# Optimization experiments

Hardware: AMD Instinct MI355X
Metric: run time of the kernel (lower is better)

The kernel has to match this reference:

```python
import jax, jax.numpy as jnp
import numpy as np


def setup_inputs() -> dict:
    key = jax.random.key(0)
    k1, k2 = jax.random.split(key)
    # output packs [mean; diagonal_covariance] along dim 0 (torch.chunk(output, 2))
    output = jax.random.uniform(k1, (8192, 2048), dtype=jnp.float32, minval=0.05, maxval=1.0)
    target = jax.random.uniform(k2, (4096, 2048), dtype=jnp.float32)
    return {"output": output, "target": target}


def reference(output, target):
    mean, diag_cov = jnp.split(output, 2, axis=0)          # each [B, D]
    mean_err = mean - target
    # logdet(diagflat(cov)) == sum(log(cov)) over ALL entries (diagflat flattens) -> scalar
    logdet = jnp.sum(jnp.log(diag_cov))
    loss = mean_err * mean_err / diag_cov + logdet          # scalar broadcasts
    return -loss
```

## Files before the change

### kernel.cpp

```cpp
#include <hip/hip_runtime.h>


#define N_ELEMS (4096 * 2048)
#define N_VEC4  (N_ELEMS / 4)
#define NBLK    2048
#define NTHR    256
#define ITERS   (N_VEC4 / (NBLK * NTHR))

__global__ __launch_bounds__(256) void logdet_partial_kernel(
    const float* __restrict__ cov, float* __restrict__ partials) {
    const float4* __restrict__ c4 = reinterpret_cast<const float4*>(cov);
    int idx = blockIdx.x * blockDim.x + threadIdx.x;
    const int stride = NBLK * NTHR;

    float s = 0.0f;
    #pragma unroll
    for (int it = 0; it < ITERS; ++it) {
        float4 v = c4[idx + it * stride];
        s += __logf(v.x) + __logf(v.y) + __logf(v.z) + __logf(v.w);
    }

    #pragma unroll
    for (int off = 32; off > 0; off >>= 1)
        s += __shfl_down(s, off, 64);

    __shared__ float wsum[4];
    if ((threadIdx.x & 63) == 0) wsum[threadIdx.x >> 6] = s;
    __syncthreads();
    if (threadIdx.x == 0)
        partials[blockIdx.x] = wsum[0] + wsum[1] + wsum[2] + wsum[3];
}

__global__ __launch_bounds__(256) void nll_elem_kernel(
    const float* __restrict__ mean, const float* __restrict__ cov,
    const float* __restrict__ target, const float* __restrict__ partials,
    float* __restrict__ out) {
    const float4* __restrict__ p4 = reinterpret_cast<const float4*>(partials);
    float4 pa = p4[threadIdx.x];
    float4 pb = p4[threadIdx.x + 256];
    float s = (pa.x + pa.y) + (pa.z + pa.w) + (pb.x + pb.y) + (pb.z + pb.w);
    #pragma unroll
    for (int off = 32; off > 0; off >>= 1)
        s += __shfl_down(s, off, 64);
    __shared__ float wsum[4];
    if ((threadIdx.x & 63) == 0) wsum[threadIdx.x >> 6] = s;
    __syncthreads();
    const float logdet = (wsum[0] + wsum[1]) + (wsum[2] + wsum[3]);

    const float4* __restrict__ m4 = reinterpret_cast<const float4*>(mean);
    const float4* __restrict__ c4 = reinterpret_cast<const float4*>(cov);
    const float4* __restrict__ t4 = reinterpret_cast<const float4*>(target);
    float4* __restrict__ o4 = reinterpret_cast<float4*>(out);

    int idx = blockIdx.x * blockDim.x + threadIdx.x;
    const int stride = NBLK * NTHR;

    #pragma unroll
    for (int it = 0; it < ITERS; ++it) {
        int i = idx + it * stride;
        float4 m = m4[i];
        float4 c = c4[i];
        float4 t = t4[i];
        float4 r;
        float ex = m.x - t.x;
        float ey = m.y - t.y;
        float ez = m.z - t.z;
        float ew = m.w - t.w;
        r.x = -(ex * ex * __builtin_amdgcn_rcpf(c.x) + logdet);
        r.y = -(ey * ey * __builtin_amdgcn_rcpf(c.y) + logdet);
        r.z = -(ez * ez * __builtin_amdgcn_rcpf(c.z) + logdet);
        r.w = -(ew * ew * __builtin_amdgcn_rcpf(c.w) + logdet);
        o4[i] = r;
    }
}

extern "C" void kernel_launch(void* const* d_in, const int* in_sizes, int n_in,
                              void* d_out, int out_size, void* d_ws, size_t ws_size,
                              hipStream_t stream) {
    const float* output = (const float*)d_in[0];
    const float* target = (const float*)d_in[1];
    const float* mean = output;
    const float* cov  = output + N_ELEMS;
    float* out = (float*)d_out;
    float* partials = (float*)d_ws;

    logdet_partial_kernel<<<NBLK, NTHR, 0, stream>>>(cov, partials);
    nll_elem_kernel<<<NBLK, NTHR, 0, stream>>>(mean, cov, target, partials, out);
}
```

Before: 132.1 us.

## Fuse logdet reduction and elementwise loss into one cooperative kernel with grid sync

Replaces the two-kernel sequence with a single cooperative kernel. Each thread keeps its covariance values in registers, computes the log partial sums, and waits at a grid-wide sync. After the sync it reduces the 512 block partials and computes the output without reading the covariance from memory a second time. This removes one full pass over the 32 MB covariance half and one kernel launch. The cost is a grid barrier and higher register pressure, and the code falls back to the old two-kernel path if the cooperative launch fails.

```diff
diff --git a/kernel.cpp b/kernel.cpp
--- a/kernel.cpp
+++ b/kernel.cpp
@@ -1,37 +1,108 @@
 #include <hip/hip_runtime.h>
+#include <hip/hip_cooperative_groups.h>
 
 
 #define N_ELEMS (4096 * 2048)
 #define N_VEC4  (N_ELEMS / 4)
-#define NBLK    2048
-#define NTHR    256
-#define ITERS   (N_VEC4 / (NBLK * NTHR))
 
-__global__ __launch_bounds__(256) void logdet_partial_kernel(
+#define FNB 512
+#define FNT 512
+#define FIT (N_VEC4 / (FNB * FNT))
+
+#define BNB 2048
+#define BNT 256
+#define BIT (N_VEC4 / (BNB * BNT))
+
+__global__ __launch_bounds__(FNT, 4) void nll_fused_kernel(
+    const float* __restrict__ mean, const float* __restrict__ cov,
+    const float* __restrict__ target, float* __restrict__ partials,
+    float* __restrict__ out) {
+    const float4* __restrict__ c4 = reinterpret_cast<const float4*>(cov);
+    const int idx = blockIdx.x * FNT + threadIdx.x;
+    const int stride = FNB * FNT;
+
+    float4 cv[FIT];
+    float s = 0.0f;
+    #pragma unroll
+    for (int it = 0; it < FIT; ++it) {
+        cv[it] = c4[idx + it * stride];
+        s += __logf(cv[it].x) + __logf(cv[it].y) +
+             __logf(cv[it].z) + __logf(cv[it].w);
+    }
+    #pragma unroll
+    for (int off = 32; off > 0; off >>= 1)
+        s += __shfl_down(s, off, 64);
+    __shared__ float wsumA[FNT / 64];
+    if ((threadIdx.x & 63) == 0) wsumA[threadIdx.x >> 6] = s;
+    __syncthreads();
+    if (threadIdx.x == 0) {
+        float b = 0.0f;
+        #pragma unroll
+        for (int w = 0; w < FNT / 64; ++w) b += wsumA[w];
+        __hip_atomic_store(&partials[blockIdx.x], b,
+                           __ATOMIC_RELEASE, __HIP_MEMORY_SCOPE_AGENT);
+    }
+
+    cooperative_groups::this_grid().sync();
+
+    float p = __hip_atomic_load(&partials[threadIdx.x],
+                                __ATOMIC_RELAXED, __HIP_MEMORY_SCOPE_AGENT);
+    #pragma unroll
+    for (int off = 32; off > 0; off >>= 1)
+        p += __shfl_down(p, off, 64);
+    __shared__ float wsumB[FNT / 64];
+    if ((threadIdx.x & 63) == 0) wsumB[threadIdx.x >> 6] = p;
+    __syncthreads();
+    float logdet = 0.0f;
+    #pragma unroll
+    for (int w = 0; w < FNT / 64; ++w) logdet += wsumB[w];
+
+    const float4* __restrict__ m4 = reinterpret_cast<const float4*>(mean);
+    const float4* __restrict__ t4 = reinterpret_cast<const float4*>(target);
+    float4* __restrict__ o4 = reinterpret_cast<float4*>(out);
+    #pragma unroll
+    for (int it = 0; it < FIT; ++it) {
+        int i = idx + it * stride;
+        float4 m = m4[i];
+        float4 t = t4[i];
+        float4 c = cv[it];
+        float4 r;
+        float ex = m.x - t.x;
+        float ey = m.y - t.y;
+        float ez = m.z - t.z;
+        float ew = m.w - t.w;
+        r.x = -(ex * ex * __builtin_amdgcn_rcpf(c.x) + logdet);
+        r.y = -(ey * ey * __builtin_amdgcn_rcpf(c.y) + logdet);
+        r.z = -(ez * ez * __builtin_amdgcn_rcpf(c.z) + logdet);
+        r.w = -(ew * ew * __builtin_amdgcn_rcpf(c.w) + logdet);
+        o4[i] = r;
+    }
+}
+
+
+__global__ __launch_bounds__(BNT) void logdet_partial_kernel(
     const float* __restrict__ cov, float* __restrict__ partials) {
     const float4* __restrict__ c4 = reinterpret_cast<const float4*>(cov);
     int idx = blockIdx.x * blockDim.x + threadIdx.x;
-    const int stride = NBLK * NTHR;
+    const int stride = BNB * BNT;
 
     float s = 0.0f;
     #pragma unroll
-    for (int it = 0; it < ITERS; ++it) {
+    for (int it = 0; it < BIT; ++it) {
         float4 v = c4[idx + it * stride];
         s += __logf(v.x) + __logf(v.y) + __logf(v.z) + __logf(v.w);
     }
-
     #pragma unroll
     for (int off = 32; off > 0; off >>= 1)
         s += __shfl_down(s, off, 64);
-
     __shared__ float wsum[4];
     if ((threadIdx.x & 63) == 0) wsum[threadIdx.x >> 6] = s;
     __syncthreads();
     if (threadIdx.x == 0)
-        partials[blockIdx.x] = wsum[0] + wsum[1] + wsum[2] + wsum[3];
+        partials[blockIdx.x] = (wsum[0] + wsum[1]) + (wsum[2] + wsum[3]);
 }
 
-__global__ __launch_bounds__(256) void nll_elem_kernel(
+__global__ __launch_bounds__(BNT) void nll_elem_kernel(
     const float* __restrict__ mean, const float* __restrict__ cov,
     const float* __restrict__ target, const float* __restrict__ partials,
     float* __restrict__ out) {
@@ -53,10 +124,10 @@
     float4* __restrict__ o4 = reinterpret_cast<float4*>(out);
 
     int idx = blockIdx.x * blockDim.x + threadIdx.x;
-    const int stride = NBLK * NTHR;
+    const int stride = BNB * BNT;
 
     #pragma unroll
-    for (int it = 0; it < ITERS; ++it) {
+    for (int it = 0; it < BIT; ++it) {
         int i = idx + it * stride;
         float4 m = m4[i];
         float4 c = c4[i];
@@ -84,6 +155,14 @@
     float* out = (float*)d_out;
     float* partials = (float*)d_ws;
 
-    logdet_partial_kernel<<<NBLK, NTHR, 0, stream>>>(cov, partials);
-    nll_elem_kernel<<<NBLK, NTHR, 0, stream>>>(mean, cov, target, partials, out);
+    void* args[] = {(void*)&mean, (void*)&cov, (void*)&target,
+                    (void*)&partials, (void*)&out};
+    hipError_t e = hipLaunchCooperativeKernel((const void*)nll_fused_kernel,
+                                              dim3(FNB), dim3(FNT), args, 0,
+                                              stream);
+    if (e != hipSuccess) {
+        (void)hipGetLastError();
+        logdet_partial_kernel<<<BNB, BNT, 0, stream>>>(cov, partials);
+        nll_elem_kernel<<<BNB, BNT, 0, stream>>>(mean, cov, target, partials, out);
+    }
 }
```

Result: slower. 208.5 us (+57.9%).
